# Optimization experiments

Hardware: AMD Instinct MI355X
Metric: run time of the kernel (lower is better)

The kernel has to match this reference:

```python
import jax, jax.numpy as jnp
import numpy as np

B, S, D = 4, 2048, 512      # batch, seq, input_dim
H, HD = 8, 64               # num_heads, hidden_dim per head
O = 512                     # output_dim
NEG = jnp.float32(-1e9)     # masked_softmax fill value


def setup_inputs() -> dict:
    key = jax.random.key(0)
    ks = jax.random.split(key, 11)
    scale = 0.02
    Q = jax.random.normal(ks[0], (B, S, D), jnp.float32)
    K = jax.random.normal(ks[1], (B, S, D), jnp.float32)
    V = jax.random.normal(ks[2], (B, S, D), jnp.float32)
    mask = jnp.ones((B, S), dtype=bool)
    # Stacked per-head linear params: weight [H, D, HD], bias [H, HD]
    Wq = jax.random.normal(ks[3], (H, D, HD), jnp.float32) * scale
    bq = jax.random.normal(ks[4], (H, HD), jnp.float32) * scale
    Wk = jax.random.normal(ks[5], (H, D, HD), jnp.float32) * scale
    bk = jax.random.normal(ks[6], (H, HD), jnp.float32) * scale
    Wv = jax.random.normal(ks[7], (H, D, HD), jnp.float32) * scale
    bv = jax.random.normal(ks[8], (H, HD), jnp.float32) * scale
    Wo = jax.random.normal(ks[9], (H * HD, O), jnp.float32) * scale
    bo = jax.random.normal(ks[10], (O,), jnp.float32) * scale
    return {"Q": Q, "K": K, "V": V, "mask": mask,
            "Wq": Wq, "bq": bq, "Wk": Wk, "bk": bk,
            "Wv": Wv, "bv": bv, "Wo": Wo, "bo": bo}


def reference(Q, K, V, mask, Wq, bq, Wk, bk, Wv, bv, Wo, bo):
    # Per-head projections (vectorized over heads instead of a Python loop)
    q = jnp.einsum('bsd,hde->bhse', Q, Wq) + bq[None, :, None, :]
    k = jnp.einsum('bsd,hde->bhse', K, Wk) + bk[None, :, None, :]
    v = jnp.einsum('bsd,hde->bhse', V, Wv) + bv[None, :, None, :]
    # Scaled dot-product scores [B,H,S,S]
    scores = jnp.einsum('bhse,bhte->bhst', q, k) / jnp.sqrt(jnp.float32(HD))
    # Padding mask [b,s,t] = mask.unsqueeze(1) & mask.unsqueeze(2), then causal tril
    amask = mask[:, :, None] & mask[:, None, :]          # [B,S,S]
    causal = jnp.tril(jnp.ones((S, S), dtype=bool))
    amask = (amask & causal)[:, None, :, :]              # [B,1,S,S]
    probs = jax.nn.softmax(jnp.where(amask, scores, NEG), axis=-1)
    ctx = jnp.einsum('bhst,bhte->bhse', probs, v)        # [B,H,S,HD]
    concat = ctx.transpose(0, 2, 1, 3).reshape(B, S, H * HD)
    return concat @ Wo + bo
```

## Files before the change

### kernel.cpp

```cpp
#include <hip/hip_runtime.h>


typedef __attribute__((ext_vector_type(8))) short bf16x8;
typedef __attribute__((ext_vector_type(4))) float f32x4;
typedef unsigned short u16;

#define MFMA(a,b,c) __builtin_amdgcn_mfma_f32_16x16x32_bf16((a),(b),(c),0,0,0)

__device__ __forceinline__ u16 f2b(float f){
    union{float f;unsigned u;}v; v.f=f;
    unsigned r = v.u + 0x7fffu + ((v.u>>16)&1u);
    return (u16)(r>>16);
}

__device__ __forceinline__ void gll16(const void* g, void* l){
    __builtin_amdgcn_global_load_lds((const __attribute__((address_space(1))) unsigned int*)g,
                                     (__attribute__((address_space(3))) unsigned int*)l, 16, 0, 0);
}

__global__ __launch_bounds__(256) void prep(
    const float* __restrict__ Q, const float* __restrict__ K, const float* __restrict__ V,
    const float* __restrict__ Wq, const float* __restrict__ Wk, const float* __restrict__ Wv,
    const float* __restrict__ Wo, u16* __restrict__ wB, u16* __restrict__ xF)
{
    int z = blockIdx.z, bx = blockIdx.x, by = blockIdx.y;
    int t = threadIdx.x, w = t>>6, lane = t&63, quad = lane>>4, l16 = lane&15;
    __shared__ __align__(16) u16 xt[64][72];
    __shared__ float tile[64][68];

    if (z < 3){
        const float* X = z==0?Q:(z==1?K:V);
        int r0 = bx*64, c0 = by*64;
        int row = t>>2, cb = (t&3)*16;
        const float* sp = X + (size_t)(r0+row)*512 + c0 + cb;
        f32x4 a0=*(const f32x4*)sp, a1=*(const f32x4*)(sp+4);
        f32x4 a2=*(const f32x4*)(sp+8), a3=*(const f32x4*)(sp+12);
        bf16x8 h0, h1;
        h0[0]=(short)f2b(a0[0]); h0[1]=(short)f2b(a0[1]); h0[2]=(short)f2b(a0[2]); h0[3]=(short)f2b(a0[3]);
        h0[4]=(short)f2b(a1[0]); h0[5]=(short)f2b(a1[1]); h0[6]=(short)f2b(a1[2]); h0[7]=(short)f2b(a1[3]);
        h1[0]=(short)f2b(a2[0]); h1[1]=(short)f2b(a2[1]); h1[2]=(short)f2b(a2[2]); h1[3]=(short)f2b(a2[3]);
        h1[4]=(short)f2b(a3[0]); h1[5]=(short)f2b(a3[1]); h1[6]=(short)f2b(a3[2]); h1[7]=(short)f2b(a3[3]);
        *(bf16x8*)&xt[row][cb]   = h0;
        *(bf16x8*)&xt[row][cb+8] = h1;
        __syncthreads();
        u16* xz = xF + (size_t)z*4194304;
        #pragma unroll
        for (int ii=0; ii<2; ++ii){
            int combo = ii*4 + w, sl = combo>>1, kl = combo&1;
            bf16x8 o = *(const bf16x8*)&xt[sl*16+l16][kl*32+quad*8];
            *(bf16x8*)(xz + ((((size_t)(r0>>4)+sl)*16 + by*2 + kl)*64 + lane)*8) = o;
        }
        return;
    }
    if (bx >= 32) return;
    int wz = bx>>3, bxw = bx&7;
    {
        int kr = t>>2, c0 = (t&3)*16;
        const float* sp;
        if (wz < 3){ const float* W = wz==0?Wq:(wz==1?Wk:Wv);
            sp = W + ((size_t)bxw*512 + by*64 + kr)*64 + c0; }
        else sp = Wo + (size_t)(by*64 + kr)*512 + bxw*64 + c0;
        #pragma unroll
        for (int u=0;u<16;u+=4){ f32x4 v=*(const f32x4*)(sp+u);
            tile[kr][c0+u]=v[0]; tile[kr][c0+u+1]=v[1]; tile[kr][c0+u+2]=v[2]; tile[kr][c0+u+3]=v[3]; }
    }
    __syncthreads();
    u16* dz = wB + (size_t)wz*262144;
    #pragma unroll
    for (int ii=0; ii<2; ++ii){
        int combo = ii*4 + w, kcl = combo>>2, c16l = combo&3;
        bf16x8 o;
        #pragma unroll
        for (int j=0;j<8;++j) o[j] = (short)f2b(tile[kcl*32+quad*8+j][c16l*16+l16]);
        int kc = by*2 + kcl, c16 = bxw*4 + c16l;
        *(bf16x8*)(dz + ((size_t)(kc*32+c16)*64 + lane)*8) = o;
    }
}

__global__ __launch_bounds__(256,3) void proj5(
    const float* __restrict__ bq, const float* __restrict__ bk, const float* __restrict__ bv,
    const u16* __restrict__ wB, const u16* __restrict__ xF,
    u16* __restrict__ qF, u16* __restrict__ kF, u16* __restrict__ vF)
{
    int z = blockIdx.z, by = blockIdx.y;
    const float* bias = z==0?bq:(z==1?bk:bv);
    const u16* wz = wB + (size_t)z*262144;
    const u16* xz = xF + (size_t)z*4194304;
    int i0 = blockIdx.x*64;
    int t=threadIdx.x, w=t>>6, lane=t&63, quad=lane>>4, l16=lane&15;

    f32x4 acc[4][4];
    #pragma unroll
    for (int mr=0;mr<4;++mr)
        #pragma unroll
        for (int ec=0;ec<4;++ec) acc[mr][ec]=(f32x4){0.f,0.f,0.f,0.f};

    for (int kc=0;kc<16;++kc){
        bf16x8 af[4];
        #pragma unroll
        for (int mr=0;mr<4;++mr)
            af[mr] = *(const bf16x8*)(xz + ((((size_t)(i0>>4)+mr)*16 + kc)*64 + lane)*8);
        #pragma unroll
        for (int ec=0;ec<4;++ec){
            int c16 = by*16 + w*4 + ec;
            bf16x8 bf = *(const bf16x8*)(wz + ((size_t)(kc*32+c16)*64 + lane)*8);
            #pragma unroll
            for (int mr=0;mr<4;++mr) acc[mr][ec] = MFMA(af[mr], bf, acc[mr][ec]);
        }
    }

    __shared__ __align__(16) u16 Cs[64][264];
    float scale = (z==0)?0.125f:1.0f;
    #pragma unroll
    for (int ec=0;ec<4;++ec){
        int lc = (w*4+ec)*16 + l16;
        float bb = bias[by*256 + lc];
        #pragma unroll
        for (int mr=0;mr<4;++mr)
            #pragma unroll
            for (int r=0;r<4;++r)
                Cs[mr*16+quad*4+r][lc] = f2b((acc[mr][ec][r] + bb)*scale);
    }
    __syncthreads();
    int b = i0>>11;
    if (z < 2){
        u16* dst = (z==0) ? qF : kF;
        int sblk = (i0&2047)>>4;
        #pragma unroll
        for (int i=0;i<8;++i){
            int hl = i>>1, ec2 = i&1;
            bf16x8 v8 = *(const bf16x8*)&Cs[w*16+l16][hl*64+ec2*32+quad*8];
            int hg = by*4 + hl;
            *(bf16x8*)(dst + ((((size_t)(b*8+hg)*128 + sblk + w)*2 + ec2)*64 + lane)*8) = v8;
        }
    } else {
        int kcb = (i0&2047)>>5;
        #pragma unroll
        for (int i=0;i<8;++i){
            int c2 = w*8 + i, kcl = c2>>4, rem = c2&15, hl = rem>>2, e16 = rem&3;
            bf16x8 o;
            #pragma unroll
            for (int j=0;j<8;++j) o[j] = (short)Cs[kcl*32+quad*8+j][hl*64+e16*16+l16];
            int hg = by*4 + hl;
            *(bf16x8*)(vF + ((((size_t)(b*8+hg)*64 + kcb + kcl)*4 + e16)*64 + lane)*8) = o;
        }
    }
}

__device__ __forceinline__ void attn_body(
    int jt, int qt, int ntiles, int w, int lane, int quad, int l16,
    const u16* __restrict__ kfb, const u16* __restrict__ vfb,
    const bf16x8 (&qf)[2], const bf16x8& ones,
    bf16x8 (&kuse)[8], bf16x8 (&kload)[8],
    f32x4 (&ov)[4], f32x4& lacc, u16 (&pb)[16][72])
{
    f32x4 sv[4];
    #pragma unroll
    for (int kk=0;kk<4;++kk) sv[kk]=(f32x4){0.f,0.f,0.f,0.f};
    #pragma unroll
    for (int kk=0;kk<4;++kk)
        #pragma unroll
        for (int ec=0;ec<2;++ec)
            sv[kk] = MFMA(qf[ec], kuse[kk*2+ec], sv[kk]);
    int jn = (jt+1 < ntiles) ? jt+1 : 0;
    #pragma unroll
    for (int i=0;i<8;++i)
        kload[i] = *(const bf16x8*)(kfb + ((size_t)(jn*8+i))*512 + lane*8);
    bf16x8 vf[8];
    #pragma unroll
    for (int i=0;i<8;++i)
        vf[i] = *(const bf16x8*)(vfb + ((size_t)(jt*8+i))*512 + lane*8);
    bool diag = (jt == qt);
    #pragma unroll
    for (int kk=0;kk<4;++kk)
        #pragma unroll
        for (int r=0;r<4;++r){
            float p = __expf(sv[kk][r]);
            if (diag && (kk*16 + l16 > w*16 + quad*4 + r)) p = 0.f;
            pb[quad*4+r][kk*16+l16] = f2b(p);
        }
    #pragma unroll
    for (int kck=0;kck<2;++kck){
        bf16x8 pf = *(const bf16x8*)&pb[l16][kck*32+quad*8];
        #pragma unroll
        for (int ec=0;ec<4;++ec)
            ov[ec] = MFMA(pf, vf[kck*4+ec], ov[ec]);
        lacc = MFMA(pf, ones, lacc);
    }
}

__global__ __launch_bounds__(256,4) void attn6(
    const u16* __restrict__ qF, const u16* __restrict__ kF, const u16* __restrict__ vF,
    u16* __restrict__ concatF)
{
    int bh = blockIdx.x, slot = blockIdx.y;
    int s = slot&7, j2 = slot>>3;
    int qt = (j2==0)? s : (j2==1)? 15-s : (j2==2)? 16+s : 31-s;
    int b = bh>>3, h = bh&7;
    int t=threadIdx.x, w=t>>6, lane=t&63, quad=lane>>4, l16=lane&15;

    __shared__ __align__(16) u16 pb[4][16][72];

    const u16* kfb = kF + (size_t)bh*131072;
    const u16* vfb = vF + (size_t)bh*131072;

    bf16x8 qf[2];
    #pragma unroll
    for (int ec=0;ec<2;++ec)
        qf[ec] = *(const bf16x8*)(qF + ((((size_t)bh*128 + qt*4 + w)*2 + ec)*512) + lane*8);

    bf16x8 ones;
    { short o1 = (l16==0)?(short)0x3F80:(short)0;
      #pragma unroll
      for (int j=0;j<8;++j) ones[j]=o1; }

    f32x4 ov[4], lacc;
    #pragma unroll
    for (int ec=0;ec<4;++ec) ov[ec]=(f32x4){0.f,0.f,0.f,0.f};
    lacc=(f32x4){0.f,0.f,0.f,0.f};

    int ntiles = qt + 1;
    bf16x8 kA[8], kB[8];
    #pragma unroll
    for (int i=0;i<8;++i) kA[i] = *(const bf16x8*)(kfb + (size_t)i*512 + lane*8);

    int jt = 0;
    for (; jt+1 < ntiles; jt += 2){
        attn_body(jt,   qt, ntiles, w, lane, quad, l16, kfb, vfb, qf, ones, kA, kB, ov, lacc, pb[w]);
        attn_body(jt+1, qt, ntiles, w, lane, quad, l16, kfb, vfb, qf, ones, kB, kA, ov, lacc, pb[w]);
    }
    if (jt < ntiles)
        attn_body(jt,   qt, ntiles, w, lane, quad, l16, kfb, vfb, qf, ones, kA, kB, ov, lacc, pb[w]);

    float inv[4];
    #pragma unroll
    for (int r=0;r<4;++r) inv[r] = 1.f / __shfl(lacc[r], (lane & 48));
    #pragma unroll
    for (int ec=0;ec<4;++ec)
        #pragma unroll
        for (int r=0;r<4;++r)
            pb[w][quad*4+r][ec*16+l16] = f2b(ov[ec][r]*inv[r]);
    size_t s16 = (size_t)b*128 + qt*4 + w;
    #pragma unroll
    for (int kcl=0;kcl<2;++kcl){
        bf16x8 o = *(const bf16x8*)&pb[w][l16][kcl*32+quad*8];
        *(bf16x8*)(concatF + ((s16*16 + h*2 + kcl)*64 + lane)*8) = o;
    }
}

__global__ __launch_bounds__(256,4) void outproj5(
    const u16* __restrict__ concatF, const u16* __restrict__ WoB,
    const float* __restrict__ bo, float* __restrict__ out)
{
    int i0 = blockIdx.x*32, by = blockIdx.y;
    int t=threadIdx.x, w=t>>6, lane=t&63, quad=lane>>4, l16=lane&15;

    f32x4 acc[2][2];
    #pragma unroll
    for (int mr=0;mr<2;++mr)
        #pragma unroll
        for (int ec=0;ec<2;++ec) acc[mr][ec]=(f32x4){0.f,0.f,0.f,0.f};

    for (int kc=0;kc<16;++kc){
        bf16x8 af[2];
        #pragma unroll
        for (int mr=0;mr<2;++mr)
            af[mr] = *(const bf16x8*)(concatF + (((size_t)((i0>>4)+mr)*16 + kc)*64 + lane)*8);
        #pragma unroll
        for (int ec=0;ec<2;++ec){
            int c16 = by*8 + w*2 + ec;
            bf16x8 bf = *(const bf16x8*)(WoB + ((size_t)(kc*32+c16)*64 + lane)*8);
            #pragma unroll
            for (int mr=0;mr<2;++mr) acc[mr][ec] = MFMA(af[mr], bf, acc[mr][ec]);
        }
    }
    #pragma unroll
    for (int ec=0;ec<2;++ec){
        int col = by*128 + (w*2+ec)*16 + l16;
        float bb = bo[col];
        #pragma unroll
        for (int mr=0;mr<2;++mr)
            #pragma unroll
            for (int r=0;r<4;++r)
                out[(size_t)(i0 + mr*16 + quad*4 + r)*512 + col] = acc[mr][ec][r] + bb;
    }
}

extern "C" void kernel_launch(void* const* d_in, const int* in_sizes, int n_in,
                              void* d_out, int out_size, void* d_ws, size_t ws_size,
                              hipStream_t stream) {
    const float* Q  = (const float*)d_in[0];
    const float* K  = (const float*)d_in[1];
    const float* V  = (const float*)d_in[2];
    const float* Wq = (const float*)d_in[4];
    const float* bq = (const float*)d_in[5];
    const float* Wk = (const float*)d_in[6];
    const float* bk = (const float*)d_in[7];
    const float* Wv = (const float*)d_in[8];
    const float* bv = (const float*)d_in[9];
    const float* Wo = (const float*)d_in[10];
    const float* bo = (const float*)d_in[11];

    u16* wB      = (u16*)d_ws;
    u16* xF      = wB + (size_t)4*262144;
    u16* qF      = xF + (size_t)3*4194304;
    u16* kF      = qF + (size_t)4194304;
    u16* vF      = kF + (size_t)4194304;
    u16* concatF = vF + (size_t)4194304;

    prep<<<dim3(128,8,4), 256, 0, stream>>>(Q, K, V, Wq, Wk, Wv, Wo, wB, xF);
    proj5<<<dim3(128,2,3), 256, 0, stream>>>(bq, bk, bv, wB, xF, qF, kF, vF);
    attn6<<<dim3(32,32), 256, 0, stream>>>(qF, kF, vF, concatF);
    outproj5<<<dim3(256,4), 256, 0, stream>>>(concatF, wB + (size_t)3*262144, bo, (float*)d_out);
}
```

Baseline: 186.1 us.

## Pair causal query tiles per block so K/V loads serve two tiles

Each attention block now handles two query tiles, p and 31-p, and walks the K/V tiles once, sharing every K and V fetch between both tiles' score and PV MFMAs. This balances causal work across blocks and halves redundant K/V global reads. Probability packing now uses the v_cvt_pk_bf16_f32 instruction, and block ids are swizzled. The cost is roughly double the accumulator registers, with launch bounds lowered to 2 blocks per CU and the grid halved to 512 blocks.

```diff
diff --git a/kernel.cpp b/kernel.cpp
--- a/kernel.cpp
+++ b/kernel.cpp
@@ -11,11 +11,6 @@
     union{float f;unsigned u;}v; v.f=f;
     unsigned r = v.u + 0x7fffu + ((v.u>>16)&1u);
     return (u16)(r>>16);
-}
-
-__device__ __forceinline__ void gll16(const void* g, void* l){
-    __builtin_amdgcn_global_load_lds((const __attribute__((address_space(1))) unsigned int*)g,
-                                     (__attribute__((address_space(3))) unsigned int*)l, 16, 0, 0);
 }
 
 __global__ __launch_bounds__(256) void prep(
@@ -147,22 +142,31 @@
     }
 }
 
-__device__ __forceinline__ void attn_body(
-    int jt, int qt, int ntiles, int w, int lane, int quad, int l16,
+__device__ __forceinline__ void bodyM(
+    int jt, int qtA, int qtB, int nt, bool doA,
+    int w, int lane, int quad, int l16,
     const u16* __restrict__ kfb, const u16* __restrict__ vfb,
-    const bf16x8 (&qf)[2], const bf16x8& ones,
+    const bf16x8 (&qfA)[2], const bf16x8 (&qfB)[2], const bf16x8& ones,
     bf16x8 (&kuse)[8], bf16x8 (&kload)[8],
-    f32x4 (&ov)[4], f32x4& lacc, u16 (&pb)[16][72])
-{
-    f32x4 sv[4];
-    #pragma unroll
-    for (int kk=0;kk<4;++kk) sv[kk]=(f32x4){0.f,0.f,0.f,0.f};
+    f32x4 (&ovA)[4], f32x4& laccA, f32x4 (&ovB)[4], f32x4& laccB,
+    u16 (*pbA)[72], u16 (*pbB)[72])
+{
+    f32x4 svA[4], svB[4];
+    #pragma unroll
+    for (int kk=0;kk<4;++kk){ svA[kk]=(f32x4){0.f,0.f,0.f,0.f}; svB[kk]=(f32x4){0.f,0.f,0.f,0.f}; }
     #pragma unroll
     for (int kk=0;kk<4;++kk)
         #pragma unroll
         for (int ec=0;ec<2;++ec)
-            sv[kk] = MFMA(qf[ec], kuse[kk*2+ec], sv[kk]);
-    int jn = (jt+1 < ntiles) ? jt+1 : 0;
+            svB[kk] = MFMA(qfB[ec], kuse[kk*2+ec], svB[kk]);
+    if (doA){
+        #pragma unroll
+        for (int kk=0;kk<4;++kk)
+            #pragma unroll
+            for (int ec=0;ec<2;++ec)
+                svA[kk] = MFMA(qfA[ec], kuse[kk*2+ec], svA[kk]);
+    }
+    int jn = (jt+1 < nt) ? jt+1 : 0;
     #pragma unroll
     for (int i=0;i<8;++i)
         kload[i] = *(const bf16x8*)(kfb + ((size_t)(jn*8+i))*512 + lane*8);
@@ -170,82 +174,137 @@
     #pragma unroll
     for (int i=0;i<8;++i)
         vf[i] = *(const bf16x8*)(vfb + ((size_t)(jt*8+i))*512 + lane*8);
-    bool diag = (jt == qt);
-    #pragma unroll
-    for (int kk=0;kk<4;++kk)
-        #pragma unroll
-        for (int r=0;r<4;++r){
-            float p = __expf(sv[kk][r]);
-            if (diag && (kk*16 + l16 > w*16 + quad*4 + r)) p = 0.f;
-            pb[quad*4+r][kk*16+l16] = f2b(p);
-        }
+    if (doA){
+        bool diag = (jt == qtA);
+        #pragma unroll
+        for (int kk=0;kk<4;++kk){
+            float pv[4];
+            #pragma unroll
+            for (int r=0;r<4;++r){
+                float pe = __expf(svA[kk][r]);
+                if (diag && (kk*16 + l16 > w*16 + quad*4 + r)) pe = 0.f;
+                pv[r] = pe;
+            }
+            unsigned w01, w23;
+            asm("v_cvt_pk_bf16_f32 %0, %1, %2" : "=v"(w01) : "v"(pv[0]), "v"(pv[1]));
+            asm("v_cvt_pk_bf16_f32 %0, %1, %2" : "=v"(w23) : "v"(pv[2]), "v"(pv[3]));
+            pbA[quad*4+0][kk*16+l16] = (u16)(w01 & 0xffffu);
+            pbA[quad*4+1][kk*16+l16] = (u16)(w01 >> 16);
+            pbA[quad*4+2][kk*16+l16] = (u16)(w23 & 0xffffu);
+            pbA[quad*4+3][kk*16+l16] = (u16)(w23 >> 16);
+        }
+    }
+    {
+        bool diag = (jt == qtB);
+        #pragma unroll
+        for (int kk=0;kk<4;++kk){
+            float pv[4];
+            #pragma unroll
+            for (int r=0;r<4;++r){
+                float pe = __expf(svB[kk][r]);
+                if (diag && (kk*16 + l16 > w*16 + quad*4 + r)) pe = 0.f;
+                pv[r] = pe;
+            }
+            unsigned w01, w23;
+            asm("v_cvt_pk_bf16_f32 %0, %1, %2" : "=v"(w01) : "v"(pv[0]), "v"(pv[1]));
+            asm("v_cvt_pk_bf16_f32 %0, %1, %2" : "=v"(w23) : "v"(pv[2]), "v"(pv[3]));
+            pbB[quad*4+0][kk*16+l16] = (u16)(w01 & 0xffffu);
+            pbB[quad*4+1][kk*16+l16] = (u16)(w01 >> 16);
+            pbB[quad*4+2][kk*16+l16] = (u16)(w23 & 0xffffu);
+            pbB[quad*4+3][kk*16+l16] = (u16)(w23 >> 16);
+        }
+    }
+    if (doA){
+        #pragma unroll
+        for (int kck=0;kck<2;++kck){
+            bf16x8 pf = *(const bf16x8*)&pbA[l16][kck*32+quad*8];
+            #pragma unroll
+            for (int ec=0;ec<4;++ec)
+                ovA[ec] = MFMA(pf, vf[kck*4+ec], ovA[ec]);
+            laccA = MFMA(pf, ones, laccA);
+        }
+    }
     #pragma unroll
     for (int kck=0;kck<2;++kck){
-        bf16x8 pf = *(const bf16x8*)&pb[l16][kck*32+quad*8];
+        bf16x8 pf = *(const bf16x8*)&pbB[l16][kck*32+quad*8];
         #pragma unroll
         for (int ec=0;ec<4;++ec)
-            ov[ec] = MFMA(pf, vf[kck*4+ec], ov[ec]);
-        lacc = MFMA(pf, ones, lacc);
-    }
-}
-
-__global__ __launch_bounds__(256,4) void attn6(
+            ovB[ec] = MFMA(pf, vf[kck*4+ec], ovB[ec]);
+        laccB = MFMA(pf, ones, laccB);
+    }
+}
+
+__device__ __forceinline__ void epi(
+    int qt, int b, int h, int w, int lane, int quad, int l16,
+    f32x4 (&ov)[4], f32x4& lacc, u16 (*pbt)[72], u16* __restrict__ concatF)
+{
+    float inv[4];
+    #pragma unroll
+    for (int r=0;r<4;++r) inv[r] = 1.f / __shfl(lacc[r], (lane & 48));
+    #pragma unroll
+    for (int ec=0;ec<4;++ec)
+        #pragma unroll
+        for (int r=0;r<4;++r)
+            pbt[quad*4+r][ec*16+l16] = f2b(ov[ec][r]*inv[r]);
+    size_t s16 = (size_t)b*128 + qt*4 + w;
+    #pragma unroll
+    for (int kcl=0;kcl<2;++kcl){
+        bf16x8 o = *(const bf16x8*)&pbt[l16][kcl*32+quad*8];
+        *(bf16x8*)(concatF + ((s16*16 + h*2 + kcl)*64 + lane)*8) = o;
+    }
+}
+
+__global__ __launch_bounds__(256,2) void attn7(
     const u16* __restrict__ qF, const u16* __restrict__ kF, const u16* __restrict__ vF,
     u16* __restrict__ concatF)
 {
-    int bh = blockIdx.x, slot = blockIdx.y;
-    int s = slot&7, j2 = slot>>3;
-    int qt = (j2==0)? s : (j2==1)? 15-s : (j2==2)? 16+s : 31-s;
-    int b = bh>>3, h = bh&7;
-    int t=threadIdx.x, w=t>>6, lane=t&63, quad=lane>>4, l16=lane&15;
-
-    __shared__ __align__(16) u16 pb[4][16][72];
+    int id = blockIdx.x;
+    int swz = (id & 7)*64 + (id >> 3);
+    int bh = swz >> 4, p = swz & 15;
+    int qtA = p, qtB = 31 - p;
+    int b = bh >> 3, h = bh & 7;
+    int t = threadIdx.x, w = t>>6, lane = t&63, quad = lane>>4, l16 = lane&15;
+
+    __shared__ __align__(16) u16 pb[4][2][16][72];
 
     const u16* kfb = kF + (size_t)bh*131072;
     const u16* vfb = vF + (size_t)bh*131072;
 
-    bf16x8 qf[2];
-    #pragma unroll
-    for (int ec=0;ec<2;++ec)
-        qf[ec] = *(const bf16x8*)(qF + ((((size_t)bh*128 + qt*4 + w)*2 + ec)*512) + lane*8);
+    bf16x8 qfA[2], qfB[2];
+    #pragma unroll
+    for (int ec=0;ec<2;++ec){
+        qfA[ec] = *(const bf16x8*)(qF + ((((size_t)bh*128 + qtA*4 + w)*2 + ec)*512) + lane*8);
+        qfB[ec] = *(const bf16x8*)(qF + ((((size_t)bh*128 + qtB*4 + w)*2 + ec)*512) + lane*8);
+    }
 
     bf16x8 ones;
     { short o1 = (l16==0)?(short)0x3F80:(short)0;
       #pragma unroll
       for (int j=0;j<8;++j) ones[j]=o1; }
 
-    f32x4 ov[4], lacc;
-    #pragma unroll
-    for (int ec=0;ec<4;++ec) ov[ec]=(f32x4){0.f,0.f,0.f,0.f};
-    lacc=(f32x4){0.f,0.f,0.f,0.f};
-
-    int ntiles = qt + 1;
+    f32x4 ovA[4], ovB[4], laccA, laccB;
+    #pragma unroll
+    for (int ec=0;ec<4;++ec){ ovA[ec]=(f32x4){0.f,0.f,0.f,0.f}; ovB[ec]=(f32x4){0.f,0.f,0.f,0.f}; }
+    laccA=(f32x4){0.f,0.f,0.f,0.f}; laccB=(f32x4){0.f,0.f,0.f,0.f};
+
+    int nt = qtB + 1;
     bf16x8 kA[8], kB[8];
     #pragma unroll
     for (int i=0;i<8;++i) kA[i] = *(const bf16x8*)(kfb + (size_t)i*512 + lane*8);
 
     int jt = 0;
-    for (; jt+1 < ntiles; jt += 2){
-        attn_body(jt,   qt, ntiles, w, lane, quad, l16, kfb, vfb, qf, ones, kA, kB, ov, lacc, pb[w]);
-        attn_body(jt+1, qt, ntiles, w, lane, quad, l16, kfb, vfb, qf, ones, kB, kA, ov, lacc, pb[w]);
-    }
-    if (jt < ntiles)
-        attn_body(jt,   qt, ntiles, w, lane, quad, l16, kfb, vfb, qf, ones, kA, kB, ov, lacc, pb[w]);
-
-    float inv[4];
-    #pragma unroll
-    for (int r=0;r<4;++r) inv[r] = 1.f / __shfl(lacc[r], (lane & 48));
-    #pragma unroll
-    for (int ec=0;ec<4;++ec)
-        #pragma unroll
-        for (int r=0;r<4;++r)
-            pb[w][quad*4+r][ec*16+l16] = f2b(ov[ec][r]*inv[r]);
-    size_t s16 = (size_t)b*128 + qt*4 + w;
-    #pragma unroll
-    for (int kcl=0;kcl<2;++kcl){
-        bf16x8 o = *(const bf16x8*)&pb[w][l16][kcl*32+quad*8];
-        *(bf16x8*)(concatF + ((s16*16 + h*2 + kcl)*64 + lane)*8) = o;
-    }
+    for (; jt+1 < nt; jt += 2){
+        bodyM(jt,   qtA, qtB, nt, jt   <= qtA, w, lane, quad, l16, kfb, vfb,
+              qfA, qfB, ones, kA, kB, ovA, laccA, ovB, laccB, pb[w][0], pb[w][1]);
+        bodyM(jt+1, qtA, qtB, nt, jt+1 <= qtA, w, lane, quad, l16, kfb, vfb,
+              qfA, qfB, ones, kB, kA, ovA, laccA, ovB, laccB, pb[w][0], pb[w][1]);
+    }
+    if (jt < nt)
+        bodyM(jt,   qtA, qtB, nt, jt   <= qtA, w, lane, quad, l16, kfb, vfb,
+              qfA, qfB, ones, kA, kB, ovA, laccA, ovB, laccB, pb[w][0], pb[w][1]);
+
+    epi(qtA, b, h, w, lane, quad, l16, ovA, laccA, pb[w][0], concatF);
+    epi(qtB, b, h, w, lane, quad, l16, ovB, laccB, pb[w][1], concatF);
 }
 
 __global__ __launch_bounds__(256,4) void outproj5(
@@ -310,6 +369,6 @@
 
     prep<<<dim3(128,8,4), 256, 0, stream>>>(Q, K, V, Wq, Wk, Wv, Wo, wB, xF);
     proj5<<<dim3(128,2,3), 256, 0, stream>>>(bq, bk, bv, wB, xF, qF, kF, vF);
-    attn6<<<dim3(32,32), 256, 0, stream>>>(qF, kF, vF, concatF);
+    attn7<<<dim3(512), 256, 0, stream>>>(qF, kF, vF, concatF);
     outproj5<<<dim3(256,4), 256, 0, stream>>>(concatF, wB + (size_t)3*262144, bo, (float*)d_out);
 }
```

Result: no change. 186.4 us (+0.1%).
